# Kernel optimization log

Hardware: AMD Instinct MI355X
Metric: run time of the kernel (lower is better)

## Reference

```python
import jax, jax.numpy as jnp
import numpy as np
from jax import lax

SQRT2 = 1.4142135623730951
NEG_SLOPE = 0.2


def _haar_kernels():
    l = np.ones((1, 2), np.float32) / np.float32(np.sqrt(2.0))
    h = l.copy()
    h[0, 0] = -h[0, 0]
    ll = l.T @ l
    lh = h.T @ l
    hl = l.T @ h
    hh = h.T @ h
    return (jnp.asarray(ll), jnp.asarray(lh), jnp.asarray(hl), jnp.asarray(hh))


def _blur_kernel():
    k = np.array([1.0, 3.0, 3.0, 1.0], np.float32)
    K = np.outer(k, k)
    K /= K.sum()
    return jnp.asarray(K)


def upfirdn2d(x, kernel, up=1, down=1, pad=(0, 0, 0, 0)):
    # x: [B,C,H,W]; depthwise FIR matching StyleGAN2 upfirdn2d semantics:
    # upsample by zero-insertion (up-1 zeros AFTER each sample), pad, true
    # convolution (kernel flipped, since lax does cross-correlation), then
    # stride-`down` decimation. Trailing zeros of torch's upsampling are
    # folded into the right/bottom pad (+up-1).
    B, C, H, W = x.shape
    px0, px1, py0, py1 = pad
    w = jnp.flip(kernel, (0, 1))[None, None].astype(x.dtype)  # [1,1,kh,kw]
    y = lax.conv_general_dilated(
        x.reshape(B * C, 1, H, W), w,
        window_strides=(down, down),
        padding=((py0, py1 + up - 1), (px0, px1 + up - 1)),
        lhs_dilation=(up, up),
        dimension_numbers=('NCHW', 'OIHW', 'NCHW'))
    return y.reshape(B, C, y.shape[2], y.shape[3])


def setup_inputs() -> dict:
    key = jax.random.key(0)
    k1, k2, k3 = jax.random.split(key, 3)
    x = jax.random.normal(k1, (8, 16, 512, 512), dtype=jnp.float32)
    conv_w = jax.random.normal(k2, (512, 16, 1, 1), dtype=jnp.float32)
    conv_b = jax.random.normal(k3, (512,), dtype=jnp.float32) * 0.1
    return {"x": x, "conv_w": conv_w, "conv_b": conv_b}


def reference(x, conv_w, conv_b):
    ll, lh, hl, hh = _haar_kernels()
    # ---- InverseHaarTransform(4): 16ch [B,16,H,W] -> 4ch [B,4,2H,2W] ----
    xll, xlh, xhl, xhh = jnp.split(x, 4, axis=1)
    p = (1, 0, 1, 0)
    inv = (upfirdn2d(xll, ll, up=2, pad=p)
           + upfirdn2d(xlh, -lh, up=2, pad=p)
           + upfirdn2d(xhl, -hl, up=2, pad=p)
           + upfirdn2d(xhh, hh, up=2, pad=p))
    # ---- Downsample(blur_kernel=[1,3,3,1]): [B,4,2H,2W] -> [B,4,H,W] ----
    bk = _blur_kernel()
    pp = bk.shape[0] - 2  # p = len(kernel) - factor
    pad0, pad1 = (pp + 1) // 2, pp // 2
    dwn = upfirdn2d(inv, bk, down=2, pad=(pad0, pad1, pad0, pad1))
    # ---- HaarTransform(4): [B,4,H,W] -> [B,16,H/2,W/2] ----
    new_in = jnp.concatenate(
        [upfirdn2d(dwn, k, down=2, pad=(0, 0, 0, 0)) for k in (ll, lh, hl, hh)],
        axis=1)
    # ---- ConvLayer: EqualConv2d 1x1 (no bias) + FusedLeakyReLU ----
    fan_in = conv_w.shape[1] * conv_w.shape[2] * conv_w.shape[3]
    scale = 1.0 / float(np.sqrt(fan_in))
    out = jnp.einsum('bchw,oc->bohw', new_in, conv_w[:, :, 0, 0] * scale)
    out = out + conv_b[None, :, None, None]
    out = jnp.where(out >= 0, out, NEG_SLOPE * out) * SQRT2
    return (new_in, out)
```

## Files before the change

kernel.cpp:

```cpp
#include <hip/hip_runtime.h>


#define H_IN 512
#define W_IN 512
#define H_OUT 256
#define W_OUT 256
#define NB 8
#define C_MID 16
#define C_OUT 512

typedef float fx4 __attribute__((ext_vector_type(4)));

__device__ __forceinline__ float cL(int fsel, float a0, float a1, float a2, float a3) {
  return fsel == 0 ? (a0 + 7.f*a1 + 7.f*a2 + a3) : (a0 + a1 - a2 - a3);
}
__device__ __forceinline__ float cH(int fsel, float a0, float a1, float a2, float a3) {
  return fsel == 0 ? (a0 + 5.f*a1 - 5.f*a2 - a3) : (a0 - a1 - a2 + a3);
}

__device__ __forceinline__ fx4 vfma(fx4 v, float s, fx4 a) {
  a.x = fmaf(v.x, s, a.x); a.y = fmaf(v.y, s, a.y);
  a.z = fmaf(v.z, s, a.z); a.w = fmaf(v.w, s, a.w);
  return a;
}

__global__ __launch_bounds__(256) void k_prep(const float* __restrict__ w,
                                              const float* __restrict__ bias,
                                              float* __restrict__ wpk) {
  const int o = blockIdx.x * 256 + threadIdx.x;
  const float s2 = 1.41421356237309515f;
  const float wscale = s2 * 0.25f * (1.f / 256.f);
#pragma unroll
  for (int c = 0; c < 16; ++c) wpk[o * 32 + c] = w[o * 16 + c] * wscale;
  wpk[o * 32 + 16] = bias[o] * s2;
}

__global__ __launch_bounds__(256) void k_fused(const float* __restrict__ x,
                                               const float* __restrict__ wpk,
                                               float* __restrict__ nin,
                                               float* __restrict__ out) {
  const int t = threadIdx.x;
  const int q = t & 63;
  const int y = blockIdx.x * 4 + (t >> 6);
  const int b = blockIdx.y;
  const int y0 = 2 * y - 1;

  const float WL[2][4] = {{1.f, 7.f, 7.f, 1.f}, {1.f, 1.f, -1.f, -1.f}};
  const float WH[2][4] = {{1.f, 5.f, -5.f, -1.f}, {1.f, -1.f, -1.f, 1.f}};

  fx4 acc[16];
#pragma unroll
  for (int c = 0; c < 16; ++c) acc[c] = (fx4){0.f, 0.f, 0.f, 0.f};

#pragma unroll
  for (int ch = 0; ch < 4; ++ch) {
#pragma unroll
    for (int g = 0; g < 4; ++g) {
      const int gY = g & 1, gX = g >> 1;
      const float sg = (g == 1 || g == 2) ? -1.f : 1.f;
      const float* xp = x + (size_t)(b * 16 + g * 4 + ch) * (H_IN * W_IN);
#pragma unroll
      for (int p = 0; p < 4; ++p) {
        const int yy = y0 + p;
        if (yy < 0 || yy >= H_IN) continue;
        const float* row = xp + (size_t)yy * W_IN + 8 * q;
        const fx4 m0 = *reinterpret_cast<const fx4*>(row);
        const fx4 m1 = *reinterpret_cast<const fx4*>(row + 4);
        const float c0s = __shfl(m1.w, q - 1);
        const float c9s = __shfl(m0.x, q + 1);
        const float cc0 = (q > 0) ? c0s : 0.f;
        const float cc9 = (q < 63) ? c9s : 0.f;
        const float cc[10] = {cc0, m0.x, m0.y, m0.z, m0.w,
                              m1.x, m1.y, m1.z, m1.w, cc9};
        const float wl = sg * WL[gY][p];
        const float wh = sg * WH[gY][p];
        fx4 vL, vH;
        vL.x = cL(gX, cc[0], cc[1], cc[2], cc[3]);
        vL.y = cL(gX, cc[2], cc[3], cc[4], cc[5]);
        vL.z = cL(gX, cc[4], cc[5], cc[6], cc[7]);
        vL.w = cL(gX, cc[6], cc[7], cc[8], cc[9]);
        vH.x = cH(gX, cc[0], cc[1], cc[2], cc[3]);
        vH.y = cH(gX, cc[2], cc[3], cc[4], cc[5]);
        vH.z = cH(gX, cc[4], cc[5], cc[6], cc[7]);
        vH.w = cH(gX, cc[6], cc[7], cc[8], cc[9]);
        acc[0 * 4 + ch] = vfma(vL, wl, acc[0 * 4 + ch]);
        acc[1 * 4 + ch] = vfma(vL, wh, acc[1 * 4 + ch]);
        acc[2 * 4 + ch] = vfma(vH, wl, acc[2 * 4 + ch]);
        acc[3 * 4 + ch] = vfma(vH, wh, acc[3 * 4 + ch]);
      }
    }
  }

  const float inv = 1.f / 256.f;
#pragma unroll
  for (int c = 0; c < 16; ++c) {
    fx4 r;
    r.x = acc[c].x * inv; r.y = acc[c].y * inv;
    r.z = acc[c].z * inv; r.w = acc[c].w * inv;
    __builtin_nontemporal_store(r, reinterpret_cast<fx4*>(
        nin + ((size_t)(b * C_MID + c) * H_OUT + y) * W_OUT + 4 * q));
  }

  float* op = out + ((size_t)(b * C_OUT) * H_OUT + y) * W_OUT + 4 * q;
#pragma unroll 2
  for (int o = 0; o < C_OUT; ++o) {
    const float* __restrict__ wrow = wpk + (o << 5);
    const float bo = wrow[16];
    fx4 a; a.x = bo; a.y = bo; a.z = bo; a.w = bo;
#pragma unroll
    for (int c = 0; c < 16; ++c) a = vfma(acc[c], wrow[c], a);
    a.x = fmaxf(a.x, 0.2f * a.x);
    a.y = fmaxf(a.y, 0.2f * a.y);
    a.z = fmaxf(a.z, 0.2f * a.z);
    a.w = fmaxf(a.w, 0.2f * a.w);
    __builtin_nontemporal_store(a,
        reinterpret_cast<fx4*>(op + (size_t)o * (H_OUT * W_OUT)));
  }
}

extern "C" void kernel_launch(void* const* d_in, const int* in_sizes, int n_in,
                              void* d_out, int out_size, void* d_ws, size_t ws_size,
                              hipStream_t stream) {
  const float* x    = (const float*)d_in[0];
  const float* w    = (const float*)d_in[1];
  const float* bias = (const float*)d_in[2];
  float* nin = (float*)d_out;
  float* out = (float*)d_out + (size_t)NB * C_MID * H_OUT * W_OUT;
  float* wpk = (float*)d_ws;

  k_prep<<<dim3(2), dim3(256), 0, stream>>>(w, bias, wpk);
  k_fused<<<dim3(64, 8), dim3(256), 0, stream>>>(x, wpk, nin, out);
}
```

Before: 249.1 us.

## Process two row groups per block, overlapping next stencil loads with conv stores

Each block now handles two 4-row groups (A and B), launching half as many blocks. While row group A's 512-channel 1x1 conv output is being written, the input rows for group B are preloaded into registers one channel at a time, and B's stencil is computed in between. The goal is to hide global load latency behind the store-heavy epilogue. The cost is much higher register pressure (launch bounds set to 1 block per CU) and only 256 blocks, which is about one per CU, so occupancy falls.

```diff
diff --git a/kernel.cpp b/kernel.cpp
--- a/kernel.cpp
+++ b/kernel.cpp
@@ -35,22 +35,53 @@
   wpk[o * 32 + 16] = bias[o] * s2;
 }
 
-__global__ __launch_bounds__(256) void k_fused(const float* __restrict__ x,
-                                               const float* __restrict__ wpk,
-                                               float* __restrict__ nin,
-                                               float* __restrict__ out) {
+#define STENCIL_VISIT(m0, m1, gY, gX, sg, p, CH, ACC)                          \
+  {                                                                            \
+    const float c0s = __shfl((m1).w, q - 1);                                   \
+    const float c9s = __shfl((m0).x, q + 1);                                   \
+    const float cc0 = (q > 0) ? c0s : 0.f;                                     \
+    const float cc9 = (q < 63) ? c9s : 0.f;                                    \
+    const float wl = (sg) * WL[gY][p];                                         \
+    const float wh = (sg) * WH[gY][p];                                         \
+    fx4 vL, vH;                                                                \
+    vL.x = cL(gX, cc0,    (m0).x, (m0).y, (m0).z);                             \
+    vL.y = cL(gX, (m0).y, (m0).z, (m0).w, (m1).x);                             \
+    vL.z = cL(gX, (m0).w, (m1).x, (m1).y, (m1).z);                             \
+    vL.w = cL(gX, (m1).y, (m1).z, (m1).w, cc9);                                \
+    vH.x = cH(gX, cc0,    (m0).x, (m0).y, (m0).z);                             \
+    vH.y = cH(gX, (m0).y, (m0).z, (m0).w, (m1).x);                             \
+    vH.z = cH(gX, (m0).w, (m1).x, (m1).y, (m1).z);                             \
+    vH.w = cH(gX, (m1).y, (m1).z, (m1).w, cc9);                                \
+    ACC[0 * 4 + (CH)] = vfma(vL, wl, ACC[0 * 4 + (CH)]);                       \
+    ACC[1 * 4 + (CH)] = vfma(vL, wh, ACC[1 * 4 + (CH)]);                       \
+    ACC[2 * 4 + (CH)] = vfma(vH, wl, ACC[2 * 4 + (CH)]);                       \
+    ACC[3 * 4 + (CH)] = vfma(vH, wh, ACC[3 * 4 + (CH)]);                       \
+  }
+
+__global__ __launch_bounds__(256, 1) void k_fused(const float* __restrict__ x,
+                                                  const float* __restrict__ wpk,
+                                                  float* __restrict__ nin,
+                                                  float* __restrict__ out) {
   const int t = threadIdx.x;
   const int q = t & 63;
-  const int y = blockIdx.x * 4 + (t >> 6);
-  const int b = blockIdx.y;
-  const int y0 = 2 * y - 1;
+  const int wr = t >> 6;
+  const int bx = blockIdx.x;
+  const int b  = blockIdx.y;
 
   const float WL[2][4] = {{1.f, 7.f, 7.f, 1.f}, {1.f, 1.f, -1.f, -1.f}};
   const float WH[2][4] = {{1.f, 5.f, -5.f, -1.f}, {1.f, -1.f, -1.f, 1.f}};
 
-  fx4 acc[16];
-#pragma unroll
-  for (int c = 0; c < 16; ++c) acc[c] = (fx4){0.f, 0.f, 0.f, 0.f};
+  const int yA = (2 * bx) * 4 + wr;
+  const int yB = (2 * bx + 1) * 4 + wr;
+  const int y0A = 2 * yA - 1;
+  const int y0B = 2 * yB - 1;
+
+  fx4 accA[16], accB[16];
+#pragma unroll
+  for (int c = 0; c < 16; ++c) {
+    accA[c] = (fx4){0.f, 0.f, 0.f, 0.f};
+    accB[c] = (fx4){0.f, 0.f, 0.f, 0.f};
+  }
 
 #pragma unroll
   for (int ch = 0; ch < 4; ++ch) {
@@ -61,32 +92,12 @@
       const float* xp = x + (size_t)(b * 16 + g * 4 + ch) * (H_IN * W_IN);
 #pragma unroll
       for (int p = 0; p < 4; ++p) {
-        const int yy = y0 + p;
+        const int yy = y0A + p;
         if (yy < 0 || yy >= H_IN) continue;
         const float* row = xp + (size_t)yy * W_IN + 8 * q;
         const fx4 m0 = *reinterpret_cast<const fx4*>(row);
         const fx4 m1 = *reinterpret_cast<const fx4*>(row + 4);
-        const float c0s = __shfl(m1.w, q - 1);
-        const float c9s = __shfl(m0.x, q + 1);
-        const float cc0 = (q > 0) ? c0s : 0.f;
-        const float cc9 = (q < 63) ? c9s : 0.f;
-        const float cc[10] = {cc0, m0.x, m0.y, m0.z, m0.w,
-                              m1.x, m1.y, m1.z, m1.w, cc9};
-        const float wl = sg * WL[gY][p];
-        const float wh = sg * WH[gY][p];
-        fx4 vL, vH;
-        vL.x = cL(gX, cc[0], cc[1], cc[2], cc[3]);
-        vL.y = cL(gX, cc[2], cc[3], cc[4], cc[5]);
-        vL.z = cL(gX, cc[4], cc[5], cc[6], cc[7]);
-        vL.w = cL(gX, cc[6], cc[7], cc[8], cc[9]);
-        vH.x = cH(gX, cc[0], cc[1], cc[2], cc[3]);
-        vH.y = cH(gX, cc[2], cc[3], cc[4], cc[5]);
-        vH.z = cH(gX, cc[4], cc[5], cc[6], cc[7]);
-        vH.w = cH(gX, cc[6], cc[7], cc[8], cc[9]);
-        acc[0 * 4 + ch] = vfma(vL, wl, acc[0 * 4 + ch]);
-        acc[1 * 4 + ch] = vfma(vL, wh, acc[1 * 4 + ch]);
-        acc[2 * 4 + ch] = vfma(vH, wl, acc[2 * 4 + ch]);
-        acc[3 * 4 + ch] = vfma(vH, wh, acc[3 * 4 + ch]);
+        STENCIL_VISIT(m0, m1, gY, gX, sg, p, ch, accA);
       }
     }
   }
@@ -95,26 +106,83 @@
 #pragma unroll
   for (int c = 0; c < 16; ++c) {
     fx4 r;
-    r.x = acc[c].x * inv; r.y = acc[c].y * inv;
-    r.z = acc[c].z * inv; r.w = acc[c].w * inv;
+    r.x = accA[c].x * inv; r.y = accA[c].y * inv;
+    r.z = accA[c].z * inv; r.w = accA[c].w * inv;
     __builtin_nontemporal_store(r, reinterpret_cast<fx4*>(
-        nin + ((size_t)(b * C_MID + c) * H_OUT + y) * W_OUT + 4 * q));
-  }
-
-  float* op = out + ((size_t)(b * C_OUT) * H_OUT + y) * W_OUT + 4 * q;
+        nin + ((size_t)(b * C_MID + c) * H_OUT + yA) * W_OUT + 4 * q));
+  }
+
+  float* opA = out + ((size_t)(b * C_OUT) * H_OUT + yA) * W_OUT + 4 * q;
+#pragma unroll
+  for (int cch = 0; cch < 4; ++cch) {
+    fx4 s0[16], s1[16];
+#pragma unroll
+    for (int g = 0; g < 4; ++g) {
+      const float* xp = x + (size_t)(b * 16 + g * 4 + cch) * (H_IN * W_IN);
+#pragma unroll
+      for (int p = 0; p < 4; ++p) {
+        const int yy = y0B + p;
+        if (yy < H_IN) {
+          const float* row = xp + (size_t)yy * W_IN + 8 * q;
+          s0[g * 4 + p] = *reinterpret_cast<const fx4*>(row);
+          s1[g * 4 + p] = *reinterpret_cast<const fx4*>(row + 4);
+        } else {
+          s0[g * 4 + p] = (fx4){0.f, 0.f, 0.f, 0.f};
+          s1[g * 4 + p] = (fx4){0.f, 0.f, 0.f, 0.f};
+        }
+      }
+    }
+#pragma unroll 2
+    for (int oi = 0; oi < 128; ++oi) {
+      const int o = cch * 128 + oi;
+      const float* __restrict__ wrow = wpk + (o << 5);
+      const float bo = wrow[16];
+      fx4 a; a.x = bo; a.y = bo; a.z = bo; a.w = bo;
+#pragma unroll
+      for (int c = 0; c < 16; ++c) a = vfma(accA[c], wrow[c], a);
+      a.x = fmaxf(a.x, 0.2f * a.x);
+      a.y = fmaxf(a.y, 0.2f * a.y);
+      a.z = fmaxf(a.z, 0.2f * a.z);
+      a.w = fmaxf(a.w, 0.2f * a.w);
+      __builtin_nontemporal_store(a,
+          reinterpret_cast<fx4*>(opA + (size_t)o * (H_OUT * W_OUT)));
+    }
+#pragma unroll
+    for (int g = 0; g < 4; ++g) {
+      const int gY = g & 1, gX = g >> 1;
+      const float sg = (g == 1 || g == 2) ? -1.f : 1.f;
+#pragma unroll
+      for (int p = 0; p < 4; ++p) {
+        const fx4 m0 = s0[g * 4 + p];
+        const fx4 m1 = s1[g * 4 + p];
+        STENCIL_VISIT(m0, m1, gY, gX, sg, p, cch, accB);
+      }
+    }
+  }
+
+#pragma unroll
+  for (int c = 0; c < 16; ++c) {
+    fx4 r;
+    r.x = accB[c].x * inv; r.y = accB[c].y * inv;
+    r.z = accB[c].z * inv; r.w = accB[c].w * inv;
+    __builtin_nontemporal_store(r, reinterpret_cast<fx4*>(
+        nin + ((size_t)(b * C_MID + c) * H_OUT + yB) * W_OUT + 4 * q));
+  }
+
+  float* opB = out + ((size_t)(b * C_OUT) * H_OUT + yB) * W_OUT + 4 * q;
 #pragma unroll 2
   for (int o = 0; o < C_OUT; ++o) {
     const float* __restrict__ wrow = wpk + (o << 5);
     const float bo = wrow[16];
     fx4 a; a.x = bo; a.y = bo; a.z = bo; a.w = bo;
 #pragma unroll
-    for (int c = 0; c < 16; ++c) a = vfma(acc[c], wrow[c], a);
+    for (int c = 0; c < 16; ++c) a = vfma(accB[c], wrow[c], a);
     a.x = fmaxf(a.x, 0.2f * a.x);
     a.y = fmaxf(a.y, 0.2f * a.y);
     a.z = fmaxf(a.z, 0.2f * a.z);
     a.w = fmaxf(a.w, 0.2f * a.w);
     __builtin_nontemporal_store(a,
-        reinterpret_cast<fx4*>(op + (size_t)o * (H_OUT * W_OUT)));
+        reinterpret_cast<fx4*>(opB + (size_t)o * (H_OUT * W_OUT)));
   }
 }
 
@@ -129,5 +197,5 @@
   float* wpk = (float*)d_ws;
 
   k_prep<<<dim3(2), dim3(256), 0, stream>>>(w, bias, wpk);
-  k_fused<<<dim3(64, 8), dim3(256), 0, stream>>>(x, wpk, nin, out);
-}
+  k_fused<<<dim3(32, 8), dim3(256), 0, stream>>>(x, wpk, nin, out);
+}
```

Measured after the change: 396.3 us. 59.1% more time.
